# Performance work log

Hardware: AMD Instinct MI355X
Metric: run time of the kernel (lower is better)

The kernel has to match this reference:

```python
import jax, jax.numpy as jnp
import numpy as np

EPS = 1e-3  # tfa GroupNormalization default epsilon


def setup_inputs() -> dict:
    key = jax.random.key(0)
    ks = jax.random.split(key, 6)
    B, H, W, C = 8, 64, 64, 256
    x = jax.random.normal(ks[0], (B, H, W, C), dtype=jnp.float32)
    s = 0.05  # keep activations in a numerically sane range
    return {
        "x": x,
        "gamma": jnp.ones((C,), jnp.float32),
        "beta": jnp.zeros((C,), jnp.float32),
        "wq": jax.random.normal(ks[1], (C, C), jnp.float32) * s,
        "bq": jnp.zeros((C,), jnp.float32),
        "wk": jax.random.normal(ks[2], (C, C), jnp.float32) * s,
        "bk": jnp.zeros((C,), jnp.float32),
        "wv": jax.random.normal(ks[3], (C, C), jnp.float32) * s,
        "bv": jnp.zeros((C,), jnp.float32),
        "wp": jax.random.normal(ks[4], (C, C), jnp.float32) * s,
        "bp": jnp.zeros((C,), jnp.float32),
    }


def _group_norm1(x, gamma, beta):
    # GroupNorm with 1 group: normalize over (H, W, C) per sample,
    # per-channel affine. tfa default epsilon=1e-3.
    mean = jnp.mean(x, axis=(1, 2, 3), keepdims=True)
    var = jnp.var(x, axis=(1, 2, 3), keepdims=True)
    return (x - mean) * jax.lax.rsqrt(var + EPS) * gamma + beta


def reference(x, gamma, beta, wq, bq, wk, bk, wv, bv, wp, bp):
    B, H, W, C = x.shape
    h = _group_norm1(x, gamma, beta)
    hf = h.reshape(B, H * W, C)  # flatten spatial -> tokens
    q = hf @ wq + bq
    k = hf @ wk + bk
    v = hf @ wv + bv
    scale = jnp.float32(C) ** -0.5
    # full [B, N, N] attention scores, N = H*W (faithful to the einsum)
    scores = jnp.einsum('bnc,bmc->bnm', q, k) * scale
    attn = jax.nn.softmax(scores, axis=-1)
    o = jnp.einsum('bnm,bmc->bnc', attn, v)
    o = o @ wp + bp
    return x + o.reshape(B, H, W, C)
```

## Files before the change

### kernel.cpp

```cpp
#include <hip/hip_runtime.h>
#include <hip/hip_bf16.h>

typedef __attribute__((ext_vector_type(8))) short short8;
typedef __attribute__((ext_vector_type(4))) float f32x4;
typedef __attribute__((ext_vector_type(16))) float f32x16;
typedef long long ll_t;

#define WS_PART 0u
#define WS_STATS 4096u
#define WS_WT 8192u
#define WS_ML 532480u
#define WS_Q  2097152u
#define WS_K  (WS_Q + 16777216u)
#define WS_V  (WS_K + 16777216u)
#define WS_VT (WS_V + 16777216u)
#define WS_O  (WS_VT + 16777216u)

#define SM_C2 4.3280851f

__device__ __forceinline__ unsigned short f2bf(float f) {
  unsigned int u = __builtin_bit_cast(unsigned int, f);
  u += 0x7fffu + ((u >> 16) & 1u);
  return (unsigned short)(u >> 16);
}
__device__ __forceinline__ float bf2f(unsigned short h) {
  unsigned int u = ((unsigned int)h) << 16;
  return __builtin_bit_cast(float, u);
}
__device__ __forceinline__ unsigned char f2fp8(float f) {
  return (unsigned char)(__builtin_amdgcn_cvt_pk_fp8_f32(f, f, 0, false) & 0xff);
}

__device__ __forceinline__ void gl_lds16(const unsigned short* g, unsigned short* l) {
  __builtin_amdgcn_global_load_lds(
      (const __attribute__((address_space(1))) unsigned int*)g,
      (__attribute__((address_space(3))) unsigned int*)l, 16, 0, 0);
}

__device__ __forceinline__ f32x4 mfma_fp8(ll_t a, ll_t b, f32x4 c) {
  return __builtin_amdgcn_mfma_f32_16x16x32_fp8_fp8(a, b, c, 0, 0, 0);
}

__global__ void k_wt(const float* __restrict__ wq, const float* __restrict__ wk,
                     const float* __restrict__ wv, const float* __restrict__ wp,
                     unsigned short* __restrict__ wT) {
  int m = blockIdx.x >> 8;
  int c = blockIdx.x & 255;
  const float* w = (m == 0) ? wq : (m == 1) ? wk : (m == 2) ? wv : wp;
  int d = threadIdx.x;
  wT[(size_t)(m * 256 + d) * 256 + c] = f2bf(w[c * 256 + d]);
}

__global__ void k_gn_part(const float* __restrict__ x, float2* __restrict__ part) {
  int b = blockIdx.x >> 5, seg = blockIdx.x & 31;
  const float4* xp = (const float4*)(x + ((size_t)b << 20) + ((size_t)seg << 15));
  float s = 0.f, sq = 0.f;
  for (int i = 0; i < 32; ++i) {
    float4 v = xp[threadIdx.x + i * 256];
    s += v.x + v.y + v.z + v.w;
    sq += v.x * v.x + v.y * v.y + v.z * v.z + v.w * v.w;
  }
  for (int m = 1; m <= 32; m <<= 1) { s += __shfl_xor(s, m); sq += __shfl_xor(sq, m); }
  __shared__ float2 red[4];
  int w = threadIdx.x >> 6;
  if ((threadIdx.x & 63) == 0) red[w] = make_float2(s, sq);
  __syncthreads();
  if (threadIdx.x == 0) {
    float S = 0.f, Q = 0.f;
    for (int i = 0; i < 4; ++i) { S += red[i].x; Q += red[i].y; }
    part[blockIdx.x] = make_float2(S, Q);
  }
}

__global__ void k_gn_stats(const float2* __restrict__ part, float2* __restrict__ stats) {
  int b = blockIdx.x, t = threadIdx.x;
  float s = 0.f, sq = 0.f;
  if (t < 32) { float2 p = part[b * 32 + t]; s = p.x; sq = p.y; }
  for (int m = 1; m <= 32; m <<= 1) { s += __shfl_xor(s, m); sq += __shfl_xor(sq, m); }
  if (t == 0) {
    float mean = s * (1.f / 1048576.f);
    float var = sq * (1.f / 1048576.f) - mean * mean;
    stats[b] = make_float2(mean, rsqrtf(var + 1e-3f));
  }
}

__global__ __launch_bounds__(256) void k_qkv(
    const float* __restrict__ x, const float* __restrict__ gamma, const float* __restrict__ beta,
    const float* __restrict__ bq, const float* __restrict__ bk, const float* __restrict__ bv,
    const float2* __restrict__ stats, const unsigned short* __restrict__ wT,
    unsigned char* __restrict__ q8, unsigned char* __restrict__ k8,
    unsigned char* __restrict__ vt8)
{
  __shared__ unsigned short SMEM[16384];
  unsigned short* const As = SMEM;
  unsigned short* const Bs = SMEM + 8192;
  const int bm = blockIdx.x, bn = blockIdx.y;
  const int mat = bn >> 1, dbase = (bn & 1) * 128;
  const int tid = threadIdx.x, lane = tid & 63, w = tid >> 6;
  const int wm = w >> 1, wn = w & 1;
  const int m0 = bm * 128;
  const float2 st = stats[bm >> 5];
  f32x16 acc[2][2] = {};
  for (int ks = 0; ks < 4; ++ks) {
    for (int i = 0; i < 8; ++i) {
      int chunk = tid + i * 256;
      int row = chunk >> 4, cq = (chunk & 15) * 4;
      int c = ks * 64 + cq;
      const float4 xv = *(const float4*)(x + (size_t)(m0 + row) * 256 + c);
      const float4 g = *(const float4*)(gamma + c);
      const float4 bt = *(const float4*)(beta + c);
      unsigned short h[4];
      h[0] = f2bf((xv.x - st.x) * st.y * g.x + bt.x);
      h[1] = f2bf((xv.y - st.x) * st.y * g.y + bt.y);
      h[2] = f2bf((xv.z - st.x) * st.y * g.z + bt.z);
      h[3] = f2bf((xv.w - st.x) * st.y * g.w + bt.w);
      *(uint2*)(&As[row * 64 + (cq ^ ((row & 7) << 3))]) = *(uint2*)h;
    }
    for (int i = 0; i < 4; ++i) {
      int chunk = tid + i * 256;
      int row = chunk >> 3, cc = (chunk & 7) * 8;
      const uint4* src = (const uint4*)(wT + (size_t)(mat * 256 + dbase + row) * 256 + ks * 64 + cc);
      *(uint4*)(&Bs[row * 64 + (cc ^ ((row & 7) << 3))]) = *src;
    }
    __syncthreads();
    for (int kk = 0; kk < 4; ++kk) {
      short8 a[2], b[2];
      for (int mi = 0; mi < 2; ++mi) {
        int row = wm * 64 + mi * 32 + (lane & 31);
        int off = (kk * 16 + (lane >> 5) * 8) ^ ((row & 7) << 3);
        a[mi] = *(const short8*)(&As[row * 64 + off]);
      }
      for (int ni = 0; ni < 2; ++ni) {
        int row = wn * 64 + ni * 32 + (lane & 31);
        int off = (kk * 16 + (lane >> 5) * 8) ^ ((row & 7) << 3);
        b[ni] = *(const short8*)(&Bs[row * 64 + off]);
      }
      for (int mi = 0; mi < 2; ++mi)
        for (int ni = 0; ni < 2; ++ni)
          acc[mi][ni] = __builtin_amdgcn_mfma_f32_32x32x16_bf16(a[mi], b[ni], acc[mi][ni], 0, 0, 0);
    }
    __syncthreads();
  }
  const int batch = bm >> 5;
  if (mat == 0) {
    const float qs = 0.25f * 1.44269504f;
    for (int ni = 0; ni < 2; ++ni) {
      int dcol = dbase + wn * 64 + ni * 32 + (lane & 31);
      float bv_ = bq[dcol];
      for (int mi = 0; mi < 2; ++mi)
        for (int r = 0; r < 16; ++r) {
          int rowD = (r & 3) + 8 * (r >> 2) + 4 * (lane >> 5);
          int token = m0 + wm * 64 + mi * 32 + rowD;
          q8[(size_t)token * 256 + dcol] = f2fp8((acc[mi][ni][r] + bv_) * qs);
        }
    }
  } else if (mat == 1) {
    for (int ni = 0; ni < 2; ++ni) {
      int dcol = dbase + wn * 64 + ni * 32 + (lane & 31);
      float bv_ = bk[dcol];
      size_t cbase = (size_t)(batch * 32 + (dcol >> 3)) * 32768 + (dcol & 7);
      for (int mi = 0; mi < 2; ++mi)
        for (int r = 0; r < 16; ++r) {
          int rowD = (r & 3) + 8 * (r >> 2) + 4 * (lane >> 5);
          int token = (m0 + wm * 64 + mi * 32 + rowD) & 4095;
          k8[cbase + (size_t)token * 8] = f2fp8((acc[mi][ni][r] + bv_) * 0.25f);
        }
    }
  } else {
    unsigned char* SB = (unsigned char*)SMEM;
    for (int ni = 0; ni < 2; ++ni) {
      int dloc = wn * 64 + ni * 32 + (lane & 31);
      float bv_ = bv[dbase + dloc];
      for (int mi = 0; mi < 2; ++mi)
        for (int r = 0; r < 16; ++r) {
          int tloc = wm * 64 + mi * 32 + (r & 3) + 8 * (r >> 2) + 4 * (lane >> 5);
          SB[dloc * 128 + (tloc ^ ((dloc & 7) << 4))] = f2fp8(acc[mi][ni][r] + bv_);
        }
    }
    __syncthreads();
    const int Tbase = (bm & 31) * 16;
    for (int i2 = 0; i2 < 4; ++i2) {
      int u = tid + i2 * 256;
      int T = u >> 6;
      int dp = u & 63;
      int d0 = dp * 2;
      int tb = T * 8;
      uint2 lo = *(const uint2*)(&SB[d0 * 128 + (tb ^ ((d0 & 7) << 4))]);
      uint2 hi2 = *(const uint2*)(&SB[(d0 + 1) * 128 + (tb ^ (((d0 + 1) & 7) << 4))]);
      uint4 vv = { lo.x, lo.y, hi2.x, hi2.y };
      *(uint4*)(vt8 + ((size_t)(batch * 512 + Tbase + T) * 256 + dbase + d0) * 8) = vv;
    }
  }
}

__global__ __launch_bounds__(512, 4) void k_attn(
    const unsigned char* __restrict__ q8, const unsigned char* __restrict__ k8,
    const unsigned char* __restrict__ vt8,
    unsigned short* __restrict__ part0, unsigned short* __restrict__ part1,
    float* __restrict__ lsum)
{
  __shared__ unsigned char LDSb[65536];
  unsigned char* const Ks0 = LDSb;
  unsigned char* const Ks1 = LDSb + 16384;
  unsigned char* const Vt0 = LDSb + 32768;
  unsigned char* const Vt1 = LDSb + 49152;
  const int g = blockIdx.x & 15, qt = blockIdx.x >> 4;
  const int batch = g >> 1, half = g & 1;
  const int q0 = qt * 128;
  const int tid = threadIdx.x, lane = tid & 63, li = lane & 15, hi = lane >> 4, w = tid >> 6;

  ll_t qf8[8];
  {
    const size_t qtok = (size_t)(batch * 4096 + q0 + w * 16 + li);
#pragma unroll
    for (int kt = 0; kt < 8; ++kt)
      qf8[kt] = *(const ll_t*)(q8 + qtok * 256 + kt * 32 + hi * 8);
  }
  f32x4 acc[16] = {};
  float l_r = 0.f;
  const int idx0 = ((((hi << 1) + 0) & 3) * 16 + li) << 2;
  const int idx1 = ((((hi << 1) + 1) & 3) * 16 + li) << 2;

  unsigned kSrc[2];
  int kDst[2], vOff[2];
#pragma unroll
  for (int i = 0; i < 2; ++i) {
    kSrc[i] = (unsigned)((w * 4 + 2 * i + (lane >> 5)) * 32768 + (lane & 31) * 16);
    kDst[i] = (w * 4 + 2 * i) * 512 + lane * 16;
    vOff[i] = w * 2048 + i * 1024 + lane * 16;
  }
  const unsigned char* kb = k8 + (size_t)batch * 1048576 + half * 16384;
  const unsigned char* vb = vt8 + (size_t)batch * 1048576 + half * 524288;

#define STAGE(KD, VD) do {                                              \
    _Pragma("unroll")                                                   \
    for (int i = 0; i < 2; ++i)                                         \
      gl_lds16((const unsigned short*)(kb + kSrc[i]),                   \
               (unsigned short*)(KD + kDst[i]));                        \
    _Pragma("unroll")                                                   \
    for (int i = 0; i < 2; ++i)                                         \
      gl_lds16((const unsigned short*)(vb + vOff[i]),                   \
               (unsigned short*)(VD + vOff[i]));                        \
  } while (0)

#define QK(KVF, SDST, KC) do {                                               \
    _Pragma("unroll")                                                        \
    for (int ct = 0; ct < 2; ++ct)                                           \
      _Pragma("unroll")                                                      \
      for (int kt = 0; kt < 8; ++kt) {                                       \
        int boff = (((kt * 4 + hi) * 64) + (KVF) * 32 + ct * 16 + li) * 8;   \
        ll_t kf = *(const ll_t*)(&KC[boff]);                                 \
        SDST[ct] = mfma_fp8(kf, qf8[kt], SDST[ct]);                          \
      }                                                                      \
  } while (0)

#define SOFTMAX(SARR, PF) do {                                               \
    _Pragma("unroll")                                                        \
    for (int ct = 0; ct < 2; ++ct)                                           \
      _Pragma("unroll")                                                      \
      for (int r = 0; r < 4; ++r) {                                          \
        float p = exp2f(SARR[ct][r] - SM_C2);                                \
        SARR[ct][r] = p;                                                     \
        l_r += p;                                                            \
      }                                                                      \
    int D0 = __builtin_amdgcn_cvt_pk_fp8_f32(SARR[0][0], SARR[0][1], 0, false); \
    D0 = __builtin_amdgcn_cvt_pk_fp8_f32(SARR[0][2], SARR[0][3], D0, true);     \
    int D1 = __builtin_amdgcn_cvt_pk_fp8_f32(SARR[1][0], SARR[1][1], 0, false); \
    D1 = __builtin_amdgcn_cvt_pk_fp8_f32(SARR[1][2], SARR[1][3], D1, true);     \
    int a0 = __builtin_amdgcn_ds_bpermute(idx0, D0);                         \
    int a1 = __builtin_amdgcn_ds_bpermute(idx0, D1);                         \
    int b0 = __builtin_amdgcn_ds_bpermute(idx1, D0);                         \
    int b1 = __builtin_amdgcn_ds_bpermute(idx1, D1);                         \
    bool sel = (lane & 32) != 0;                                             \
    int2 pw = { sel ? a1 : a0, sel ? b1 : b0 };                              \
    PF = __builtin_bit_cast(ll_t, pw);                                       \
  } while (0)

#define PV(KVF, PF, VC) do {                                                 \
    __builtin_amdgcn_s_setprio(1);                                          \
    _Pragma("unroll")                                                        \
    for (int dt = 0; dt < 16; ++dt) {                                        \
      int boff = ((((KVF) * 4 + hi) * 256) + dt * 16 + li) * 8;              \
      ll_t vf = *(const ll_t*)(&VC[boff]);                                   \
      acc[dt] = mfma_fp8(PF, vf, acc[dt]);                                   \
    }                                                                        \
    __builtin_amdgcn_s_setprio(0);                                          \
  } while (0)

  STAGE(Ks0, Vt0);
  for (int it = 0; it < 32; ++it) {
    const int cur = it & 1;
    __syncthreads();
    if (it < 31) {
      kb += 512;
      vb += 16384;
      if (cur) STAGE(Ks0, Vt0); else STAGE(Ks1, Vt1);
    }
    const unsigned char* Kc = cur ? Ks1 : Ks0;
    const unsigned char* Vc = cur ? Vt1 : Vt0;

    {
      f32x4 s0[2] = {};
      __builtin_amdgcn_s_setprio(1);
      QK(0, s0, Kc);
      __builtin_amdgcn_s_setprio(0);
      ll_t pf0;
      SOFTMAX(s0, pf0);
      PV(0, pf0, Vc);
    }
    {
      f32x4 s1[2] = {};
      __builtin_amdgcn_s_setprio(1);
      QK(1, s1, Kc);
      __builtin_amdgcn_s_setprio(0);
      ll_t pf1;
      SOFTMAX(s1, pf1);
      PV(1, pf1, Vc);
    }
  }
#undef STAGE
#undef QK
#undef SOFTMAX
#undef PV
  l_r += __shfl_xor(l_r, 16);
  l_r += __shfl_xor(l_r, 32);
  __syncthreads();
  if (lane < 16)
    lsum[half * 32768 + (size_t)batch * 4096 + q0 + w * 16 + lane] = l_r;
  unsigned short* Lw = (unsigned short*)LDSb + w * 4096;
#pragma unroll
  for (int dt = 0; dt < 16; ++dt)
#pragma unroll
    for (int r = 0; r < 4; ++r)
      Lw[(hi * 4 + r) * 256 + dt * 16 + li] = f2bf(acc[dt][r]);
  unsigned short* pout = (half ? part1 : part0) + ((size_t)batch * 4096 + q0 + w * 16) * 256;
#pragma unroll
  for (int i = 0; i < 8; ++i) {
    short8 v = *(const short8*)(&Lw[i * 512 + lane * 8]);
    int row = i * 2 + (lane >> 5);
    *(short8*)(pout + row * 256 + (lane & 31) * 8) = v;
  }
}

__global__ __launch_bounds__(256) void k_proj(
    const unsigned short* __restrict__ p0, const unsigned short* __restrict__ p1,
    const float* __restrict__ lsum, const unsigned short* __restrict__ wT,
    const float* __restrict__ bp, const float* __restrict__ x, float* __restrict__ out)
{
  __shared__ unsigned short As[128 * 64];
  __shared__ unsigned short Bs[128 * 64];
  const int bm = blockIdx.x, bn = blockIdx.y;
  const int dbase = bn * 128;
  const int tid = threadIdx.x, lane = tid & 63, w = tid >> 6;
  const int wm = w >> 1, wn = w & 1;
  const int m0 = bm * 128;
  f32x16 acc[2][2] = {};
  for (int ks = 0; ks < 4; ++ks) {
    for (int i = 0; i < 4; ++i) {
      int chunk = tid + i * 256;
      int row = chunk >> 3, cc = (chunk & 7) * 8;
      int tok = m0 + row;
      float r = 1.f / (lsum[tok] + lsum[32768 + tok]);
      short8 u0 = *(const short8*)(p0 + (size_t)tok * 256 + ks * 64 + cc);
      short8 u1 = *(const short8*)(p1 + (size_t)tok * 256 + ks * 64 + cc);
      unsigned short hh[8];
      for (int j = 0; j < 8; ++j)
        hh[j] = f2bf(r * (bf2f((unsigned short)u0[j]) + bf2f((unsigned short)u1[j])));
      *(uint4*)(&As[row * 64 + (cc ^ ((row & 7) << 3))]) = *(uint4*)hh;
    }
    for (int i = 0; i < 4; ++i) {
      int chunk = tid + i * 256;
      int row = chunk >> 3, cc = (chunk & 7) * 8;
      const uint4* src = (const uint4*)(wT + (size_t)(3 * 256 + dbase + row) * 256 + ks * 64 + cc);
      *(uint4*)(&Bs[row * 64 + (cc ^ ((row & 7) << 3))]) = *src;
    }
    __syncthreads();
    for (int kk = 0; kk < 4; ++kk) {
      short8 a[2], b[2];
      for (int mi = 0; mi < 2; ++mi) {
        int row = wm * 64 + mi * 32 + (lane & 31);
        int off = (kk * 16 + (lane >> 5) * 8) ^ ((row & 7) << 3);
        a[mi] = *(const short8*)(&As[row * 64 + off]);
      }
      for (int ni = 0; ni < 2; ++ni) {
        int row = wn * 64 + ni * 32 + (lane & 31);
        int off = (kk * 16 + (lane >> 5) * 8) ^ ((row & 7) << 3);
        b[ni] = *(const short8*)(&Bs[row * 64 + off]);
      }
      for (int mi = 0; mi < 2; ++mi)
        for (int ni = 0; ni < 2; ++ni)
          acc[mi][ni] = __builtin_amdgcn_mfma_f32_32x32x16_bf16(a[mi], b[ni], acc[mi][ni], 0, 0, 0);
    }
    __syncthreads();
  }
  for (int ni = 0; ni < 2; ++ni) {
    int dcol = dbase + wn * 64 + ni * 32 + (lane & 31);
    float bv_ = bp[dcol];
    for (int mi = 0; mi < 2; ++mi)
      for (int r = 0; r < 16; ++r) {
        int rowD = (r & 3) + 8 * (r >> 2) + 4 * (lane >> 5);
        size_t idx = (size_t)(m0 + wm * 64 + mi * 32 + rowD) * 256 + dcol;
        out[idx] = x[idx] + acc[mi][ni][r] + bv_;
      }
  }
}

extern "C" void kernel_launch(void* const* d_in, const int* in_sizes, int n_in,
                              void* d_out, int out_size, void* d_ws, size_t ws_size,
                              hipStream_t stream) {
  const float* x = (const float*)d_in[0];
  const float* gamma = (const float*)d_in[1];
  const float* beta = (const float*)d_in[2];
  const float* wq = (const float*)d_in[3];
  const float* bq = (const float*)d_in[4];
  const float* wk = (const float*)d_in[5];
  const float* bk = (const float*)d_in[6];
  const float* wv = (const float*)d_in[7];
  const float* bv = (const float*)d_in[8];
  const float* wp = (const float*)d_in[9];
  const float* bp = (const float*)d_in[10];
  char* ws = (char*)d_ws;
  float2* part = (float2*)(ws + WS_PART);
  float2* stats = (float2*)(ws + WS_STATS);
  unsigned short* wT = (unsigned short*)(ws + WS_WT);
  float* lsw = (float*)(ws + WS_ML);
  unsigned char* q8 = (unsigned char*)(ws + WS_Q);
  unsigned char* k8 = (unsigned char*)(ws + WS_K);
  unsigned short* vw = (unsigned short*)(ws + WS_V);
  unsigned char* vt8 = (unsigned char*)(ws + WS_VT);
  unsigned short* ow = (unsigned short*)(ws + WS_O);
  float* out = (float*)d_out;

  k_wt<<<1024, 256, 0, stream>>>(wq, wk, wv, wp, wT);
  k_gn_part<<<256, 256, 0, stream>>>(x, part);
  k_gn_stats<<<8, 64, 0, stream>>>(part, stats);
  k_qkv<<<dim3(256, 6), 256, 0, stream>>>(x, gamma, beta, bq, bk, bv, stats, wT, q8, k8, vt8);
  k_attn<<<512, 512, 0, stream>>>(q8, k8, vt8, vw, ow, lsw);
  k_proj<<<dim3(256, 2), 256, 0, stream>>>(vw, ow, lsw, wT, bp, x, out);
}
```

Baseline: 183.2 us.

## Use 16x16x128 scaled FP8 MFMA for QK and fold GN stats into QKV kernel

The QK^T product in the attention kernel now uses the gfx950 scaled MFMA 16x16x128 f8f6f4 instruction with unit scales. Each 16-column tile takes two instructions instead of eight 16x16x32 FP8 MFMAs, and Q fragments are loaded as wide 32-byte vectors. Separately, the tiny k_gn_stats launch is removed: each k_qkv block reduces the 32 partial sums itself and shares the result through LDS. This trades one kernel launch for redundant per-block work, and it relies on the K-operand LDS layout lining up with the new instruction's lane mapping.

```diff
diff --git a/kernel.cpp b/kernel.cpp
--- a/kernel.cpp
+++ b/kernel.cpp
@@ -4,10 +4,10 @@
 typedef __attribute__((ext_vector_type(8))) short short8;
 typedef __attribute__((ext_vector_type(4))) float f32x4;
 typedef __attribute__((ext_vector_type(16))) float f32x16;
+typedef __attribute__((ext_vector_type(8))) int i32x8;
 typedef long long ll_t;
 
 #define WS_PART 0u
-#define WS_STATS 4096u
 #define WS_WT 8192u
 #define WS_ML 532480u
 #define WS_Q  2097152u
@@ -72,26 +72,15 @@
   }
 }
 
-__global__ void k_gn_stats(const float2* __restrict__ part, float2* __restrict__ stats) {
-  int b = blockIdx.x, t = threadIdx.x;
-  float s = 0.f, sq = 0.f;
-  if (t < 32) { float2 p = part[b * 32 + t]; s = p.x; sq = p.y; }
-  for (int m = 1; m <= 32; m <<= 1) { s += __shfl_xor(s, m); sq += __shfl_xor(sq, m); }
-  if (t == 0) {
-    float mean = s * (1.f / 1048576.f);
-    float var = sq * (1.f / 1048576.f) - mean * mean;
-    stats[b] = make_float2(mean, rsqrtf(var + 1e-3f));
-  }
-}
-
 __global__ __launch_bounds__(256) void k_qkv(
     const float* __restrict__ x, const float* __restrict__ gamma, const float* __restrict__ beta,
     const float* __restrict__ bq, const float* __restrict__ bk, const float* __restrict__ bv,
-    const float2* __restrict__ stats, const unsigned short* __restrict__ wT,
+    const float2* __restrict__ part, const unsigned short* __restrict__ wT,
     unsigned char* __restrict__ q8, unsigned char* __restrict__ k8,
     unsigned char* __restrict__ vt8)
 {
   __shared__ unsigned short SMEM[16384];
+  __shared__ float2 stSh;
   unsigned short* const As = SMEM;
   unsigned short* const Bs = SMEM + 8192;
   const int bm = blockIdx.x, bn = blockIdx.y;
@@ -99,7 +88,18 @@
   const int tid = threadIdx.x, lane = tid & 63, w = tid >> 6;
   const int wm = w >> 1, wn = w & 1;
   const int m0 = bm * 128;
-  const float2 st = stats[bm >> 5];
+  if (tid < 32) {
+    float2 p = part[(bm >> 5) * 32 + tid];
+    float s = p.x, sq = p.y;
+    for (int m = 1; m <= 16; m <<= 1) { s += __shfl_xor(s, m); sq += __shfl_xor(sq, m); }
+    if (tid == 0) {
+      float mean = s * (1.f / 1048576.f);
+      float var = sq * (1.f / 1048576.f) - mean * mean;
+      stSh = make_float2(mean, rsqrtf(var + 1e-3f));
+    }
+  }
+  __syncthreads();
+  const float2 st = stSh;
   f32x16 acc[2][2] = {};
   for (int ks = 0; ks < 4; ++ks) {
     for (int i = 0; i < 8; ++i) {
@@ -209,12 +209,17 @@
   const int q0 = qt * 128;
   const int tid = threadIdx.x, lane = tid & 63, li = lane & 15, hi = lane >> 4, w = tid >> 6;
 
-  ll_t qf8[8];
+  i32x8 qm0, qm1;
   {
-    const size_t qtok = (size_t)(batch * 4096 + q0 + w * 16 + li);
-#pragma unroll
-    for (int kt = 0; kt < 8; ++kt)
-      qf8[kt] = *(const ll_t*)(q8 + qtok * 256 + kt * 32 + hi * 8);
+    const unsigned char* qp = q8 + ((size_t)(batch * 4096 + q0 + w * 16 + li)) * 256 + hi * 32;
+    uint4 a = *(const uint4*)(qp);
+    uint4 b = *(const uint4*)(qp + 16);
+    qm0 = (i32x8){(int)a.x, (int)a.y, (int)a.z, (int)a.w,
+                  (int)b.x, (int)b.y, (int)b.z, (int)b.w};
+    uint4 c = *(const uint4*)(qp + 128);
+    uint4 d = *(const uint4*)(qp + 144);
+    qm1 = (i32x8){(int)c.x, (int)c.y, (int)c.z, (int)c.w,
+                  (int)d.x, (int)d.y, (int)d.z, (int)d.w};
   }
   f32x4 acc[16] = {};
   float l_r = 0.f;
@@ -243,15 +248,26 @@
                (unsigned short*)(VD + vOff[i]));                        \
   } while (0)
 
+#define QKT(T, SDST, KC) do {                                                \
+    i32x8 a0, a1;                                                            \
+    _Pragma("unroll")                                                        \
+    for (int p = 0; p < 4; ++p) {                                            \
+      ll_t r0 = *(const ll_t*)(&KC[(((4 * hi + p) * 64) + (T) * 16 + li) * 8]);      \
+      ll_t r1 = *(const ll_t*)(&KC[(((16 + 4 * hi + p) * 64) + (T) * 16 + li) * 8]); \
+      int2 u0 = __builtin_bit_cast(int2, r0);                                \
+      int2 u1 = __builtin_bit_cast(int2, r1);                                \
+      a0[2 * p] = u0.x; a0[2 * p + 1] = u0.y;                                \
+      a1[2 * p] = u1.x; a1[2 * p + 1] = u1.y;                                \
+    }                                                                        \
+    SDST = __builtin_amdgcn_mfma_scale_f32_16x16x128_f8f6f4(                 \
+        a0, qm0, SDST, 0, 0, 0, 127, 0, 127);                                \
+    SDST = __builtin_amdgcn_mfma_scale_f32_16x16x128_f8f6f4(                 \
+        a1, qm1, SDST, 0, 0, 0, 127, 0, 127);                                \
+  } while (0)
+
 #define QK(KVF, SDST, KC) do {                                               \
-    _Pragma("unroll")                                                        \
-    for (int ct = 0; ct < 2; ++ct)                                           \
-      _Pragma("unroll")                                                      \
-      for (int kt = 0; kt < 8; ++kt) {                                       \
-        int boff = (((kt * 4 + hi) * 64) + (KVF) * 32 + ct * 16 + li) * 8;   \
-        ll_t kf = *(const ll_t*)(&KC[boff]);                                 \
-        SDST[ct] = mfma_fp8(kf, qf8[kt], SDST[ct]);                          \
-      }                                                                      \
+    QKT(2 * (KVF) + 0, SDST[0], KC);                                         \
+    QKT(2 * (KVF) + 1, SDST[1], KC);                                         \
   } while (0)
 
 #define SOFTMAX(SARR, PF) do {                                               \
@@ -319,6 +335,7 @@
     }
   }
 #undef STAGE
+#undef QKT
 #undef QK
 #undef SOFTMAX
 #undef PV
@@ -421,7 +438,6 @@
   const float* bp = (const float*)d_in[10];
   char* ws = (char*)d_ws;
   float2* part = (float2*)(ws + WS_PART);
-  float2* stats = (float2*)(ws + WS_STATS);
   unsigned short* wT = (unsigned short*)(ws + WS_WT);
   float* lsw = (float*)(ws + WS_ML);
   unsigned char* q8 = (unsigned char*)(ws + WS_Q);
@@ -433,8 +449,7 @@
 
   k_wt<<<1024, 256, 0, stream>>>(wq, wk, wv, wp, wT);
   k_gn_part<<<256, 256, 0, stream>>>(x, part);
-  k_gn_stats<<<8, 64, 0, stream>>>(part, stats);
-  k_qkv<<<dim3(256, 6), 256, 0, stream>>>(x, gamma, beta, bq, bk, bv, stats, wT, q8, k8, vt8);
+  k_qkv<<<dim3(256, 6), 256, 0, stream>>>(x, gamma, beta, bq, bk, bv, part, wT, q8, k8, vt8);
   k_attn<<<512, 512, 0, stream>>>(q8, k8, vt8, vw, ow, lsw);
   k_proj<<<dim3(256, 2), 256, 0, stream>>>(vw, ow, lsw, wT, bp, x, out);
 }
```

Measured after the change: 436.6 us. +138.3%, slower.
